# Kernel tuning notes

Hardware: AMD Instinct MI355X
Metric: run time of the kernel (lower is better)

Reference implementation:

```python
import jax, jax.numpy as jnp
import numpy as np

M, IN, OUT = 8192, 4096, 4096
BLOCK_N, BLOCK_K = 128, 128
NB = IN // BLOCK_K  # 32 in-blocks
INT8_MAX = 127.0
EPS = 1e-6


def setup_inputs() -> dict:
    key = jax.random.key(0)
    k1, k2, k3, k4 = jax.random.split(key, 4)
    x = jax.random.normal(k1, (M, IN), dtype=jnp.float32)
    # pre-quantized int8 weights, layout [output_size, input_size]
    weight_q = jax.random.randint(k2, (OUT, IN), -128, 128, dtype=jnp.int8)
    # block-wise scales, kernel-ready layout [in_blocks, 1, output_size]
    weight_scale = (jax.random.uniform(k3, (NB, 1, OUT), dtype=jnp.float32) + 0.5) * 0.01
    bias = jax.random.normal(k4, (OUT,), dtype=jnp.float32)
    return {"x": x, "weight_q": weight_q, "weight_scale": weight_scale, "bias": bias}


def _quantize_activation(x):
    # dynamic per-token symmetric int8 quantization
    amax = jnp.max(jnp.abs(x), axis=-1, keepdims=True)          # [M, 1]
    x_scale = jnp.maximum(amax, EPS) / INT8_MAX                  # [M, 1]
    x_q = jnp.clip(jnp.round(x / x_scale), -128.0, 127.0)        # [M, IN]
    return x_q, x_scale


def reference(x, weight_q, weight_scale, bias):
    # x: [M, IN]; weight_q: [OUT, IN] int8; weight_scale: [NB, 1, OUT]; bias: [OUT]
    x_q, x_scale = _quantize_activation(x)
    # Dequantize weights block-wise along K: scale for column k, row n is
    # weight_scale[k // BLOCK_K, 0, n].
    ws = weight_scale[:, 0, :].T                                 # [OUT, NB]
    w_deq = (weight_q.astype(jnp.float32).reshape(OUT, NB, BLOCK_K)
             * ws[:, :, None]).reshape(OUT, IN)                  # [OUT, IN] fp32
    # quantized matmul + dequant by activation scale
    out = jnp.einsum('mk,nk->mn', x_q, w_deq) * x_scale          # [M, OUT]
    out = out + bias
    return out
```

## Files before the change

kernel.cpp:

```cpp
#include <hip/hip_runtime.h>
#include <cstdint>

#define M_DIM 8192
#define K_DIM 4096
#define N_DIM 4096
#define NKT   32

typedef int   v4i __attribute__((ext_vector_type(4)));
typedef float v4f __attribute__((ext_vector_type(4)));

__device__ __forceinline__ void gload_lds16(const void* g, void* l) {
  __builtin_amdgcn_global_load_lds(
      (const __attribute__((address_space(1))) void*)g,
      (__attribute__((address_space(3))) void*)l, 16, 0, 0);
}

__global__ __launch_bounds__(256) void pack_w(
    const int* __restrict__ w32, int* __restrict__ w8) {
  const size_t i = (size_t)blockIdx.x * 256 + threadIdx.x;
  const int4 v = ((const int4*)w32)[i];
  w8[i] = (v.x & 255) | ((v.y & 255) << 8) | ((v.z & 255) << 16) | ((v.w & 255) << 24);
}

__global__ __launch_bounds__(256) void quant_rows(
    const float* __restrict__ x, int8_t* __restrict__ xq, float* __restrict__ xs) {
  const int row = blockIdx.x;
  const int tid = threadIdx.x;
  const float4* xr = (const float4*)(x + (size_t)row * K_DIM);

  float4 v[4];
  float amax = 0.f;
#pragma unroll
  for (int i = 0; i < 4; ++i) {
    v[i] = xr[i * 256 + tid];
    amax = fmaxf(amax, fmaxf(fmaxf(fabsf(v[i].x), fabsf(v[i].y)),
                             fmaxf(fabsf(v[i].z), fabsf(v[i].w))));
  }
#pragma unroll
  for (int off = 32; off > 0; off >>= 1)
    amax = fmaxf(amax, __shfl_xor(amax, off, 64));

  __shared__ float red[4];
  if ((tid & 63) == 0) red[tid >> 6] = amax;
  __syncthreads();
  amax = fmaxf(fmaxf(red[0], red[1]), fmaxf(red[2], red[3]));
  amax = fmaxf(amax, 1e-6f);
  const float s   = amax / 127.0f;
  const float inv = 127.0f / amax;
  if (tid == 0) xs[row] = s;

  int* xqo = (int*)(xq + (size_t)row * K_DIM);
#pragma unroll
  for (int i = 0; i < 4; ++i) {
    int q0 = (int)fminf(fmaxf(rintf(v[i].x * inv), -128.f), 127.f);
    int q1 = (int)fminf(fmaxf(rintf(v[i].y * inv), -128.f), 127.f);
    int q2 = (int)fminf(fmaxf(rintf(v[i].z * inv), -128.f), 127.f);
    int q3 = (int)fminf(fmaxf(rintf(v[i].w * inv), -128.f), 127.f);
    xqo[i * 256 + tid] =
        (q0 & 255) | ((q1 & 255) << 8) | ((q2 & 255) << 16) | ((q3 & 255) << 24);
  }
}

__global__ __launch_bounds__(512, 2) void gemm_q8(
    const int8_t* __restrict__ xq, const int8_t* __restrict__ wq,
    const float* __restrict__ wscale, const float* __restrict__ xs,
    const float* __restrict__ bias, float* __restrict__ out) {
  __shared__ int8_t lA[2][32768];
  __shared__ int8_t lB[2][32768];

  const int tid = threadIdx.x;
  const int m0 = blockIdx.x * 256;
  const int n0 = blockIdx.y * 256;

  const int srow   = tid >> 3;
  const int schunk = (tid & 7) ^ (srow & 7);
  const int8_t* ga = xq + (size_t)(m0 + srow) * K_DIM + schunk * 16;
  const int8_t* gb = wq + (size_t)(n0 + srow) * K_DIM + schunk * 16;

  const int lane = tid & 63;
  const int wv = tid >> 6;
  const int wm = (wv >> 2) << 7;
  const int wn = (wv & 3) << 6;
  const int lr = lane & 15;
  const int lq = lane >> 4;

  const int swz0 = ((lq ^ (lr & 7)) << 4);
  const int swz1 = (((4 | lq) ^ (lr & 7)) << 4);
  const int arow = (wm + lr) << 7;
  const int brow = (wn + lr) << 7;

  v4f facc[8][4];
#pragma unroll
  for (int i = 0; i < 8; ++i)
#pragma unroll
    for (int j = 0; j < 4; ++j) facc[i][j] = {0.f, 0.f, 0.f, 0.f};

  const float* wsp = wscale + n0 + wn + lr;

#pragma unroll
  for (int h = 0; h < 2; ++h)
#pragma unroll
    for (int p = 0; p < 2; ++p) {
      const size_t go = (size_t)(h * 128 + p * 64) * K_DIM;
      const int lo = h * 16384 + p * 8192 + tid * 16;
      gload_lds16(ga + go, &lA[0][lo]);
      gload_lds16(gb + go, &lB[0][lo]);
    }
  asm volatile("s_waitcnt vmcnt(0)" ::: "memory");
  __builtin_amdgcn_s_barrier();

  for (int kt = 0; kt < NKT; ++kt) {
    const int d = kt & 1;
    const int kn = (kt + 1) & (NKT - 1);
    const int8_t* gan = ga + (size_t)kn * 128;
    const int8_t* gbn = gb + (size_t)kn * 128;
    int8_t* lan = &lA[d ^ 1][0];
    int8_t* lbn = &lB[d ^ 1][0];
    const int8_t* pa0 = &lA[d][arow + swz0];
    const int8_t* pa1 = &lA[d][arow + swz1];
    const int8_t* pb0 = &lB[d][brow + swz0];
    const int8_t* pb1 = &lB[d][brow + swz1];

    float wsv[4];
#pragma unroll
    for (int j = 0; j < 4; ++j) wsv[j] = wsp[(size_t)kt * N_DIM + j * 16];

#pragma unroll
    for (int q = 0; q < 4; ++q) {
      v4i af[2][2], bf[4][2];
#pragma unroll
      for (int ii = 0; ii < 2; ++ii) {
        af[ii][0] = *(const v4i*)(pa0 + (q * 2 + ii) * 2048);
        af[ii][1] = *(const v4i*)(pa1 + (q * 2 + ii) * 2048);
      }
#pragma unroll
      for (int j = 0; j < 4; ++j) {
        bf[j][0] = *(const v4i*)(pb0 + j * 2048);
        bf[j][1] = *(const v4i*)(pb1 + j * 2048);
      }

      if (q < 2) {
#pragma unroll
        for (int p = 0; p < 2; ++p) {
          const size_t go = (size_t)(q * 128 + p * 64) * K_DIM;
          const int lo = q * 16384 + p * 8192 + tid * 16;
          gload_lds16(gan + go, lan + lo);
          gload_lds16(gbn + go, lbn + lo);
        }
      }

      __builtin_amdgcn_s_barrier();
      asm volatile("s_waitcnt lgkmcnt(0)" ::: "memory");
      __builtin_amdgcn_sched_barrier(0);

      __builtin_amdgcn_s_setprio(1);
      v4i ic[2][4];
#pragma unroll
      for (int ii = 0; ii < 2; ++ii)
#pragma unroll
        for (int j = 0; j < 4; ++j) {
          ic[ii][j] = {0, 0, 0, 0};
          ic[ii][j] = __builtin_amdgcn_mfma_i32_16x16x64_i8(af[ii][0], bf[j][0], ic[ii][j], 0, 0, 0);
          ic[ii][j] = __builtin_amdgcn_mfma_i32_16x16x64_i8(af[ii][1], bf[j][1], ic[ii][j], 0, 0, 0);
        }
      __builtin_amdgcn_s_setprio(0);

#pragma unroll
      for (int ii = 0; ii < 2; ++ii)
#pragma unroll
        for (int j = 0; j < 4; ++j)
#pragma unroll
          for (int r = 0; r < 4; ++r)
            facc[q * 2 + ii][j][r] += wsv[j] * (float)ic[ii][j][r];

      if (q == 3) {
        asm volatile("s_waitcnt vmcnt(0)" ::: "memory");
        __builtin_amdgcn_sched_barrier(0);
      }
      __builtin_amdgcn_s_barrier();
    }
  }

  float bv[4];
#pragma unroll
  for (int j = 0; j < 4; ++j) bv[j] = bias[n0 + wn + j * 16 + lr];
#pragma unroll
  for (int i = 0; i < 8; ++i) {
    const int mb = m0 + wm + i * 16 + (lq << 2);
#pragma unroll
    for (int r = 0; r < 4; ++r) {
      const float sc = xs[mb + r];
      float* op = out + (size_t)(mb + r) * N_DIM + n0 + wn + lr;
#pragma unroll
      for (int j = 0; j < 4; ++j) op[j * 16] = facc[i][j][r] * sc + bv[j];
    }
  }
}

extern "C" void kernel_launch(void* const* d_in, const int* in_sizes, int n_in,
                              void* d_out, int out_size, void* d_ws, size_t ws_size,
                              hipStream_t stream) {
  const float* x      = (const float*)d_in[0];
  const int*   w32    = (const int*)d_in[1];
  const float* wscale = (const float*)d_in[2];
  const float* bias   = (const float*)d_in[3];
  float* out = (float*)d_out;

  int8_t* xq  = (int8_t*)d_ws;
  int8_t* wq8 = (int8_t*)d_ws + (size_t)M_DIM * K_DIM;
  float*  xs  = (float*)((char*)d_ws + (size_t)M_DIM * K_DIM + (size_t)N_DIM * K_DIM);

  pack_w<<<(N_DIM * (size_t)K_DIM / 4 + 255) / 256, 256, 0, stream>>>(w32, (int*)wq8);
  quant_rows<<<M_DIM, 256, 0, stream>>>(x, xq, xs);
  dim3 grid(M_DIM / 256, N_DIM / 256);
  gemm_q8<<<grid, 512, 0, stream>>>(xq, wq8, wscale, xs, bias, out);
}
```

Before: 465.6 us.

## Switch int8 GEMM to 32x32x32 MFMA with register-prefetched A fragments

Replaces the 16x16x64 int8 MFMA tiling with 32x32x32 MFMA tiles, so each wave computes 4x2 tiles of 32x32 and the per-block scale dequant runs on 16-element accumulators. The loop is restructured so B fragments are loaded once per k-tile, A fragments are double-buffered in registers, and all next-tile global-to-LDS loads are issued up front. The per-quarter barriers are replaced by one __syncthreads per k-tile. The aim is fewer LDS reads per MFMA and less synchronisation overhead. The trade-off is more accumulator register pressure and less fine-grained overlap between loads and compute.

Measured after the change: 440.0 us. 1.06x faster.

```diff
diff --git a/kernel.cpp b/kernel.cpp
--- a/kernel.cpp
+++ b/kernel.cpp
@@ -6,8 +6,9 @@
 #define N_DIM 4096
 #define NKT   32
 
-typedef int   v4i __attribute__((ext_vector_type(4)));
-typedef float v4f __attribute__((ext_vector_type(4)));
+typedef int   v4i  __attribute__((ext_vector_type(4)));
+typedef int   v16i __attribute__((ext_vector_type(16)));
+typedef float v4f  __attribute__((ext_vector_type(4)));
 
 __device__ __forceinline__ void gload_lds16(const void* g, void* l) {
   __builtin_amdgcn_global_load_lds(
@@ -78,24 +79,27 @@
   const int8_t* gb = wq + (size_t)(n0 + srow) * K_DIM + schunk * 16;
 
   const int lane = tid & 63;
-  const int wv = tid >> 6;
-  const int wm = (wv >> 2) << 7;
-  const int wn = (wv & 3) << 6;
-  const int lr = lane & 15;
-  const int lq = lane >> 4;
-
-  const int swz0 = ((lq ^ (lr & 7)) << 4);
-  const int swz1 = (((4 | lq) ^ (lr & 7)) << 4);
-  const int arow = (wm + lr) << 7;
-  const int brow = (wn + lr) << 7;
-
-  v4f facc[8][4];
-#pragma unroll
-  for (int i = 0; i < 8; ++i)
-#pragma unroll
-    for (int j = 0; j < 4; ++j) facc[i][j] = {0.f, 0.f, 0.f, 0.f};
-
-  const float* wsp = wscale + n0 + wn + lr;
+  const int wv  = tid >> 6;
+  const int wm  = (wv >> 2) << 7;
+  const int wn  = (wv & 3) << 6;
+  const int l31 = lane & 31;
+  const int hi  = lane >> 5;
+
+  int swz[4];
+#pragma unroll
+  for (int k = 0; k < 4; ++k) swz[k] = (((2 * k + hi) ^ (lane & 7)) << 4);
+  const int aoff = (wm + l31) << 7;
+  const int boff = (wn + l31) << 7;
+
+  float facc[4][2][16];
+#pragma unroll
+  for (int i = 0; i < 4; ++i)
+#pragma unroll
+    for (int j = 0; j < 2; ++j)
+#pragma unroll
+      for (int r = 0; r < 16; ++r) facc[i][j][r] = 0.f;
+
+  const float* wsp = wscale + n0 + wn + l31;
 
 #pragma unroll
   for (int h = 0; h < 2; ++h)
@@ -106,8 +110,7 @@
       gload_lds16(ga + go, &lA[0][lo]);
       gload_lds16(gb + go, &lB[0][lo]);
     }
-  asm volatile("s_waitcnt vmcnt(0)" ::: "memory");
-  __builtin_amdgcn_s_barrier();
+  __syncthreads();
 
   for (int kt = 0; kt < NKT; ++kt) {
     const int d = kt & 1;
@@ -116,83 +119,82 @@
     const int8_t* gbn = gb + (size_t)kn * 128;
     int8_t* lan = &lA[d ^ 1][0];
     int8_t* lbn = &lB[d ^ 1][0];
-    const int8_t* pa0 = &lA[d][arow + swz0];
-    const int8_t* pa1 = &lA[d][arow + swz1];
-    const int8_t* pb0 = &lB[d][brow + swz0];
-    const int8_t* pb1 = &lB[d][brow + swz1];
-
-    float wsv[4];
-#pragma unroll
-    for (int j = 0; j < 4; ++j) wsv[j] = wsp[(size_t)kt * N_DIM + j * 16];
-
+    const int8_t* pa = &lA[d][0];
+    const int8_t* pb = &lB[d][0];
+
+    const float ws0 = wsp[(size_t)kt * N_DIM];
+    const float ws1 = wsp[(size_t)kt * N_DIM + 32];
+
+    v4i bfr[2][4];
+#pragma unroll
+    for (int j = 0; j < 2; ++j)
+#pragma unroll
+      for (int k = 0; k < 4; ++k)
+        bfr[j][k] = *(const v4i*)(pb + boff + j * 4096 + swz[k]);
+
+    v4i acur[4];
+#pragma unroll
+    for (int k = 0; k < 4; ++k)
+      acur[k] = *(const v4i*)(pa + aoff + swz[k]);
+
+#pragma unroll
+    for (int h = 0; h < 2; ++h)
+#pragma unroll
+      for (int p = 0; p < 2; ++p) {
+        const size_t go = (size_t)(h * 128 + p * 64) * K_DIM;
+        const int lo = h * 16384 + p * 8192 + tid * 16;
+        gload_lds16(gan + go, lan + lo);
+        gload_lds16(gbn + go, lbn + lo);
+      }
+
+#pragma unroll
+    for (int i = 0; i < 4; ++i) {
+      v4i anxt[4];
+      if (i < 3) {
+#pragma unroll
+        for (int k = 0; k < 4; ++k)
+          anxt[k] = *(const v4i*)(pa + aoff + (i + 1) * 4096 + swz[k]);
+      }
+
+      v16i ic0 = {};
+      v16i ic1 = {};
+      __builtin_amdgcn_s_setprio(1);
+#pragma unroll
+      for (int k = 0; k < 4; ++k) {
+        ic0 = __builtin_amdgcn_mfma_i32_32x32x32_i8(acur[k], bfr[0][k], ic0, 0, 0, 0);
+        ic1 = __builtin_amdgcn_mfma_i32_32x32x32_i8(acur[k], bfr[1][k], ic1, 0, 0, 0);
+      }
+      __builtin_amdgcn_s_setprio(0);
+
+#pragma unroll
+      for (int r = 0; r < 16; ++r) facc[i][0][r] += ws0 * (float)ic0[r];
+#pragma unroll
+      for (int r = 0; r < 16; ++r) facc[i][1][r] += ws1 * (float)ic1[r];
+
+      if (i < 3) {
+#pragma unroll
+        for (int k = 0; k < 4; ++k) acur[k] = anxt[k];
+      }
+    }
+
+    __syncthreads();
+  }
+
+  const float bv0 = bias[n0 + wn + l31];
+  const float bv1 = bias[n0 + wn + 32 + l31];
+#pragma unroll
+  for (int i = 0; i < 4; ++i) {
+    const int rbase = m0 + wm + i * 32 + (hi << 2);
 #pragma unroll
     for (int q = 0; q < 4; ++q) {
-      v4i af[2][2], bf[4][2];
-#pragma unroll
-      for (int ii = 0; ii < 2; ++ii) {
-        af[ii][0] = *(const v4i*)(pa0 + (q * 2 + ii) * 2048);
-        af[ii][1] = *(const v4i*)(pa1 + (q * 2 + ii) * 2048);
-      }
-#pragma unroll
-      for (int j = 0; j < 4; ++j) {
-        bf[j][0] = *(const v4i*)(pb0 + j * 2048);
-        bf[j][1] = *(const v4i*)(pb1 + j * 2048);
-      }
-
-      if (q < 2) {
-#pragma unroll
-        for (int p = 0; p < 2; ++p) {
-          const size_t go = (size_t)(q * 128 + p * 64) * K_DIM;
-          const int lo = q * 16384 + p * 8192 + tid * 16;
-          gload_lds16(gan + go, lan + lo);
-          gload_lds16(gbn + go, lbn + lo);
-        }
-      }
-
-      __builtin_amdgcn_s_barrier();
-      asm volatile("s_waitcnt lgkmcnt(0)" ::: "memory");
-      __builtin_amdgcn_sched_barrier(0);
-
-      __builtin_amdgcn_s_setprio(1);
-      v4i ic[2][4];
-#pragma unroll
-      for (int ii = 0; ii < 2; ++ii)
-#pragma unroll
-        for (int j = 0; j < 4; ++j) {
-          ic[ii][j] = {0, 0, 0, 0};
-          ic[ii][j] = __builtin_amdgcn_mfma_i32_16x16x64_i8(af[ii][0], bf[j][0], ic[ii][j], 0, 0, 0);
-          ic[ii][j] = __builtin_amdgcn_mfma_i32_16x16x64_i8(af[ii][1], bf[j][1], ic[ii][j], 0, 0, 0);
-        }
-      __builtin_amdgcn_s_setprio(0);
-
-#pragma unroll
-      for (int ii = 0; ii < 2; ++ii)
-#pragma unroll
-        for (int j = 0; j < 4; ++j)
-#pragma unroll
-          for (int r = 0; r < 4; ++r)
-            facc[q * 2 + ii][j][r] += wsv[j] * (float)ic[ii][j][r];
-
-      if (q == 3) {
-        asm volatile("s_waitcnt vmcnt(0)" ::: "memory");
-        __builtin_amdgcn_sched_barrier(0);
-      }
-      __builtin_amdgcn_s_barrier();
-    }
-  }
-
-  float bv[4];
-#pragma unroll
-  for (int j = 0; j < 4; ++j) bv[j] = bias[n0 + wn + j * 16 + lr];
-#pragma unroll
-  for (int i = 0; i < 8; ++i) {
-    const int mb = m0 + wm + i * 16 + (lq << 2);
-#pragma unroll
-    for (int r = 0; r < 4; ++r) {
-      const float sc = xs[mb + r];
-      float* op = out + (size_t)(mb + r) * N_DIM + n0 + wn + lr;
-#pragma unroll
-      for (int j = 0; j < 4; ++j) op[j * 16] = facc[i][j][r] * sc + bv[j];
+      const v4f xv = *(const v4f*)(xs + rbase + q * 8);
+#pragma unroll
+      for (int r4 = 0; r4 < 4; ++r4) {
+        const int r = q * 4 + r4;
+        float* op = out + (size_t)(rbase + q * 8 + r4) * N_DIM + n0 + wn + l31;
+        op[0]  = facc[i][0][r] * xv[r4] + bv0;
+        op[32] = facc[i][1][r] * xv[r4] + bv1;
+      }
     }
   }
 }
```
